# Optimization experiments

Hardware: AMD Instinct MI355X
Metric: run time of the kernel (lower is better)

## Reference

```python
import jax, jax.numpy as jnp
import numpy as np

K = 20  # max object ids (ids 1..K); masks value 0 = background
EPS_GN = 1e-5

def _conv3(x, w, b):
    # 3x3 conv, padding=1 == SAME, NCHW/OIHW
    y = jax.lax.conv_general_dilated(x, w, (1, 1), 'SAME',
                                     dimension_numbers=('NCHW', 'OIHW', 'NCHW'))
    return y + b[None, :, None, None]

def _groupnorm(x, groups, w, b):
    B, C, H, W = x.shape
    xg = x.reshape(B, groups, C // groups, H, W)
    m = xg.mean(axis=(2, 3, 4), keepdims=True)
    v = xg.var(axis=(2, 3, 4), keepdims=True)
    xn = ((xg - m) * jax.lax.rsqrt(v + EPS_GN)).reshape(B, C, H, W)
    return xn * w[None, :, None, None] + b[None, :, None, None]


def setup_inputs() -> dict:
    key = jax.random.key(0)
    ks = jax.random.split(key, 8)
    def p(k, shape, s=0.05):
        return jax.random.normal(k, shape, jnp.float32) * s
    return {
        'x': jax.random.normal(ks[0], (4, 512, 128, 128), jnp.float32),
        'masks': jax.random.randint(ks[1], (4, 128, 128), 0, 21, jnp.int32),
        'w1': p(ks[2], (256, 512, 3, 3)), 'b1': jnp.zeros((256,), jnp.float32),
        'g1w': jnp.ones((256,), jnp.float32), 'g1b': jnp.zeros((256,), jnp.float32),
        'w2': p(ks[3], (128, 256, 3, 3)), 'b2': jnp.zeros((128,), jnp.float32),
        'g2w': jnp.ones((128,), jnp.float32), 'g2b': jnp.zeros((128,), jnp.float32),
        'w3': p(ks[4], (64, 128, 3, 3)), 'b3': jnp.zeros((64,), jnp.float32),
        'g3w': jnp.ones((64,), jnp.float32), 'g3b': jnp.zeros((64,), jnp.float32),
        'wb': p(ks[5], (7, 64)), 'bb': jnp.zeros((7,), jnp.float32),
        'wc': p(ks[6], (1, 64)), 'bc': jnp.zeros((1,), jnp.float32),
    }


def reference(x, masks, w1, b1, g1w, g1b, w2, b2, g2w, g2b,
              w3, b3, g3w, g3b, wb, bb, wc, bc):
    # encoder: (conv3 -> GN -> relu) x3
    h = jax.nn.relu(_groupnorm(_conv3(x, w1, b1), 8, g1w, g1b))
    h = jax.nn.relu(_groupnorm(_conv3(h, w2, b2), 4, g2w, g2b))
    h = jax.nn.relu(_groupnorm(_conv3(h, w3, b3), 4, g3w, g3b))  # [B,64,H,W]

    # masked segment-mean pooling over all ids 1..K (vectorized unique-loop)
    ids = jnp.arange(1, K + 1, dtype=masks.dtype)
    onehot = (masks[:, None, :, :] == ids[None, :, None, None]).astype(h.dtype)  # [B,K,H,W]
    sums = jnp.einsum('bchw,bkhw->bkc', h, onehot)          # [B,K,64]
    counts = onehot.sum(axis=(2, 3))                        # [B,K]
    pooled = sums / (counts[..., None] + 1e-6)              # [B,K,64]

    # 1x1 conv heads on pooled vector == dense matmuls
    boxes = jnp.einsum('bkc,oc->bko', pooled, wb) + bb      # [B,K,7]
    scores = jax.nn.sigmoid(jnp.einsum('bkc,oc->bko', pooled, wc) + bc)[..., 0]  # [B,K]
    return (boxes, scores)
```

## Files before the change

### kernel.cpp

```cpp
#include <hip/hip_runtime.h>
#include <hip/hip_bf16.h>
#include <math.h>

#define HW 16384
#define BATCH 4
#define KIDS 20

using short8 = __attribute__((ext_vector_type(8))) short;
using f32x4  = __attribute__((ext_vector_type(4))) float;

__device__ __forceinline__ unsigned short bfbits(float f) {
  __hip_bfloat16 h = __float2bfloat16(f);
  return *(unsigned short*)&h;
}

__device__ __forceinline__ void gload_lds16(const void* g, void* l) {
  __builtin_amdgcn_global_load_lds(
      (const __attribute__((address_space(1))) void*)g,
      (__attribute__((address_space(3))) void*)l, 16, 0, 0);
}

__global__ __launch_bounds__(256) void zero_k(float* __restrict__ p, int n) {
  int i = blockIdx.x*256 + threadIdx.x;
  if (i < n) p[i] = 0.f;
}

__global__ __launch_bounds__(256) void x_to_nhwc_k(const float* __restrict__ in,
                                                   __hip_bfloat16* __restrict__ out)
{
  __shared__ float tile[32][65];
  int t = blockIdx.x;
  const int pxt = t & 255; t >>= 8;
  const int ct  = t & 15;  t >>= 4;
  const int b   = t;
  const int tid = threadIdx.x;
  #pragma unroll
  for (int it = 0; it < 8; ++it) {
    int idx = tid + it*256;
    int px_l = idx & 63, c_l = idx >> 6;
    tile[c_l][px_l] = in[((size_t)(b*512 + ct*32 + c_l))*HW + pxt*64 + px_l];
  }
  __syncthreads();
  #pragma unroll
  for (int it = 0; it < 4; ++it) {
    int idx = tid + it*256;
    int c2 = idx & 15, px_l = idx >> 4;
    unsigned u = ((unsigned)bfbits(tile[c2*2+1][px_l]) << 16) | bfbits(tile[c2*2][px_l]);
    *(unsigned*)(out + ((size_t)(b*HW + pxt*64 + px_l))*512 + ct*32 + c2*2) = u;
  }
}

template<int Co, int Ci>
__global__ __launch_bounds__(256) void pack_w_k(const float* __restrict__ w,
                                                __hip_bfloat16* __restrict__ out)
{
  const int i = blockIdx.x*256 + threadIdx.x;
  const int ci = i & (Ci-1);
  const int r  = i >> __builtin_ctz(Ci);
  const int co = r & (Co-1);
  const int t  = r >> __builtin_ctz(Co);
  out[i] = __float2bfloat16(w[((size_t)co*Ci + ci)*9 + t]);
}

template<int Ci, int Co, int CPG, int MT>
__global__ __launch_bounds__(512, 2) void conv_mfma_k(
    const __hip_bfloat16* __restrict__ xin,
    const __hip_bfloat16* __restrict__ wpk,
    const float* __restrict__ bias,
    float* __restrict__ out,
    float* __restrict__ partS, float* __restrict__ partSS)
{
  constexpr int ROWS = 2, NT = 4, SR = 4, RG = 64;
  constexpr int WCO = 2*MT*16;
  constexpr int NC  = Ci/32;
  constexpr int NGW = (MT*16)/CPG;
  constexpr int IB  = SR*130*32;
  constexpr int UW  = 9*WCO/16;
  __shared__ __align__(16) short lds[2*IB + 9*WCO*32];
  short* const wlds = lds + 2*IB;

  const int b  = blockIdx.x / RG;
  const int r0 = (blockIdx.x % RG) * ROWS;
  const int co0 = blockIdx.y * WCO;
  const int tid = threadIdx.x;
  const int wave = tid >> 6, lane = tid & 63;
  const int row_w = wave & 1;
  const int pw    = (wave >> 1) & 1;
  const int coh   = wave >> 2;
  const int co_w  = co0 + coh*MT*16;
  const int y = r0 + row_w;
  const int lr = lane & 15, q = lane >> 4;
  const int ls = lane >> 2, lq = lane & 3;

  if (tid < 64) {
    int q16 = tid & 3, u = tid >> 2;
    int side = u & 1, r = (u >> 1) & 3, buf = u >> 3;
    short8 z = {0,0,0,0,0,0,0,0};
    *(short8*)(lds + buf*IB + (r*130 + (side ? 129 : 0))*32 + q16*8) = z;
  }
  if (r0 == 0) {
    short8 z = {0,0,0,0,0,0,0,0};
    for (int i = tid; i < 2*520; i += 512) {
      int buf = i / 520, j = i % 520;
      *((short8*)(lds + buf*IB) + j) = z;
    }
  }
  if (r0 == 126) {
    short8 z = {0,0,0,0,0,0,0,0};
    for (int i = tid; i < 2*520; i += 512) {
      int buf = i / 520, j = i % 520;
      *((short8*)(lds + buf*IB + (SR-1)*130*32) + j) = z;
    }
  }

  const size_t in_base = (size_t)b * HW * Ci;
  auto stage_i = [&](int buf, int ci0) {
    #pragma unroll
    for (int it = 0; it < 4; ++it) {
      int gi = wave*4 + it;
      int r = gi >> 3, seg = gi & 7;
      int yy = r0 + r - 1;
      if ((unsigned)yy < 128u)
        gload_lds16(xin + in_base + (size_t)(yy*128 + seg*16 + ls)*Ci + ci0 + lq*8,
                    lds + buf*IB + (r*130 + seg*16 + 1)*32);
    }
  };
  auto stage_w = [&](int ci0) {
    for (int u = wave; u < UW; u += 8) {
      int t = u / (WCO/16), cb = u % (WCO/16);
      gload_lds16(wpk + ((size_t)(t*Co + co0 + cb*16 + ls))*Ci + ci0 + lq*8,
                  wlds + (t*WCO + cb*16)*32);
    }
  };

  f32x4 acc[MT][NT] = {};
  stage_i(0, 0);
  __syncthreads();
  int cur = 0;
  for (int c = 0; c < NC; ++c) {
    const int ci0 = c*32;
    stage_w(ci0);
    if (c+1 < NC) {
      stage_i(cur^1, ci0 + 32);
      asm volatile("s_waitcnt vmcnt(4)" ::: "memory");
    } else {
      asm volatile("s_waitcnt vmcnt(0)" ::: "memory");
    }
    __builtin_amdgcn_s_barrier();
    __builtin_amdgcn_sched_barrier(0);
    const short* ib = lds + cur*IB;
    #pragma unroll
    for (int t = 0; t < 9; ++t) {
      const int dy = t/3, dx = t%3;
      short8 af[MT], bf[NT];
      #pragma unroll
      for (int mt = 0; mt < MT; ++mt)
        af[mt] = *(const short8*)(wlds + (t*WCO + coh*MT*16 + mt*16 + lr)*32 + q*8);
      #pragma unroll
      for (int nt = 0; nt < NT; ++nt)
        bf[nt] = *(const short8*)(ib + ((row_w+dy)*130 + pw*64 + nt*16 + lr + dx)*32 + q*8);
      #pragma unroll
      for (int mt = 0; mt < MT; ++mt)
        #pragma unroll
        for (int nt = 0; nt < NT; ++nt)
          acc[mt][nt] = __builtin_amdgcn_mfma_f32_16x16x32_bf16(
              af[mt], bf[nt], acc[mt][nt], 0, 0, 0);
    }
    __builtin_amdgcn_s_barrier();
    cur ^= 1;
  }

  float sg[NGW] = {}, ssg[NGW] = {};
  #pragma unroll
  for (int mt = 0; mt < MT; ++mt) {
    const int g = (mt*16) / CPG;
    #pragma unroll
    for (int nt = 0; nt < NT; ++nt) {
      int px = pw*64 + nt*16 + lr;
      int co = co_w + mt*16 + q*4;
      const float4 bv = *(const float4*)(bias + co);
      f32x4 v = acc[mt][nt];
      v[0] += bv.x; v[1] += bv.y; v[2] += bv.z; v[3] += bv.w;
      sg[g]  += v[0] + v[1] + v[2] + v[3];
      ssg[g] += v[0]*v[0] + v[1]*v[1] + v[2]*v[2] + v[3]*v[3];
      *(f32x4*)(out + ((size_t)(b*HW + y*128 + px))*Co + co) = v;
    }
  }
  const int bgbase = b*(Co/CPG) + co_w/CPG;
  #pragma unroll
  for (int g = 0; g < NGW; ++g) {
    float s = sg[g], ss = ssg[g];
    #pragma unroll
    for (int off = 32; off; off >>= 1) {
      s  += __shfl_xor(s, off);
      ss += __shfl_xor(ss, off);
    }
    if (lane == 0) {
      atomicAdd(&partS[bgbase + g], s);
      atomicAdd(&partSS[bgbase + g], ss);
    }
  }
}

__global__ void gn_final_k(const float* __restrict__ partS,
                           const float* __restrict__ partSS,
                           float* __restrict__ mv, int nbg, float inv_n)
{
  const int i = threadIdx.x;
  if (i < nbg) {
    float s = partS[i], ss = partSS[i];
    float mean = s*inv_n, var = ss*inv_n - mean*mean;
    mv[2*i] = mean; mv[2*i+1] = rsqrtf(var + 1e-5f);
  }
}

template<int C, int CPG, bool BF16OUT>
__global__ __launch_bounds__(256) void gn_apply_k(const float* __restrict__ in,
    const float* __restrict__ mv, const float* __restrict__ gw,
    const float* __restrict__ gb, void* __restrict__ outp)
{
  constexpr int C4 = C/4;
  constexpr int G = C/CPG;
  const int i = blockIdx.x*256 + threadIdx.x;
  const int c4 = i & (C4-1);
  const int pxb = i >> __builtin_ctz(C4);
  const int b = pxb >> 14;
  const int c = c4*4;
  const int bg = b*G + c/CPG;
  const float mean = mv[2*bg], inv = mv[2*bg+1];
  float4 v = *((const float4*)in + i);
  const float4 w4 = *(const float4*)(gw + c);
  const float4 b4 = *(const float4*)(gb + c);
  float r0 = fmaxf((v.x-mean)*inv*w4.x + b4.x, 0.f);
  float r1 = fmaxf((v.y-mean)*inv*w4.y + b4.y, 0.f);
  float r2 = fmaxf((v.z-mean)*inv*w4.z + b4.z, 0.f);
  float r3 = fmaxf((v.w-mean)*inv*w4.w + b4.w, 0.f);
  if (BF16OUT) {
    uint2 o;
    o.x = ((unsigned)bfbits(r1) << 16) | bfbits(r0);
    o.y = ((unsigned)bfbits(r3) << 16) | bfbits(r2);
    *(uint2*)((__hip_bfloat16*)outp + (size_t)i*4) = o;
  } else {
    *((float4*)outp + i) = make_float4(r0,r1,r2,r3);
  }
}

__global__ __launch_bounds__(256) void pool_counts_k(
    const int* __restrict__ masks, float* __restrict__ counts)
{
  __shared__ int hist[KIDS];
  const int b = blockIdx.x;
  if (threadIdx.x < KIDS) hist[threadIdx.x] = 0;
  __syncthreads();
  for (int p = threadIdx.x; p < HW; p += 256) {
    const int m = masks[b*HW + p];
    if (m > 0) atomicAdd(&hist[m-1], 1);
  }
  __syncthreads();
  if (threadIdx.x < KIDS) counts[b*KIDS + threadIdx.x] = (float)hist[threadIdx.x];
}

__global__ __launch_bounds__(256) void pool_sums_k(const float* __restrict__ h3,
    const int* __restrict__ masks, float* __restrict__ sums)
{
  __shared__ float acc[KIDS*64];
  const int b = blockIdx.x >> 5, chunk = blockIdx.x & 31;
  const int tid = threadIdx.x;
  for (int j = tid; j < KIDS*64; j += 256) acc[j] = 0.f;
  __syncthreads();
  const int ch = tid & 63, pi = tid >> 6;
  const int p0 = chunk*512;
  for (int p = p0 + pi; p < p0 + 512; p += 4) {
    int m = masks[b*HW + p];
    if (m > 0) atomicAdd(&acc[(m-1)*64 + ch], h3[((size_t)(b*HW + p))*64 + ch]);
  }
  __syncthreads();
  for (int j = tid; j < KIDS*64; j += 256) atomicAdd(&sums[b*KIDS*64 + j], acc[j]);
}

__global__ __launch_bounds__(64) void heads_k(
    const float* __restrict__ sums, const float* __restrict__ counts,
    const float* __restrict__ wb, const float* __restrict__ bb,
    const float* __restrict__ wc, const float* __restrict__ bc,
    float* __restrict__ out)
{
  const int bk = blockIdx.x;
  const int c = threadIdx.x;
  const float pooled = sums[bk*64 + c] / (counts[bk] + 1e-6f);
  #pragma unroll
  for (int o = 0; o < 7; ++o) {
    float t = pooled * wb[o*64 + c];
    for (int off = 32; off > 0; off >>= 1) t += __shfl_down(t, off);
    if (c == 0) out[bk*7 + o] = t + bb[o];
  }
  float t = pooled * wc[c];
  for (int off = 32; off > 0; off >>= 1) t += __shfl_down(t, off);
  if (c == 0) out[BATCH*KIDS*7 + bk] = 1.f / (1.f + expf(-(t + bc[0])));
}

extern "C" void kernel_launch(void* const* d_in, const int* in_sizes, int n_in,
                              void* d_out, int out_size, void* d_ws, size_t ws_size,
                              hipStream_t stream)
{
  const float* x     = (const float*)d_in[0];
  const int*   masks = (const int*)  d_in[1];
  const float* w1 = (const float*)d_in[2];
  const float* b1 = (const float*)d_in[3];
  const float* g1w= (const float*)d_in[4];
  const float* g1b= (const float*)d_in[5];
  const float* w2 = (const float*)d_in[6];
  const float* b2 = (const float*)d_in[7];
  const float* g2w= (const float*)d_in[8];
  const float* g2b= (const float*)d_in[9];
  const float* w3 = (const float*)d_in[10];
  const float* b3 = (const float*)d_in[11];
  const float* g3w= (const float*)d_in[12];
  const float* g3b= (const float*)d_in[13];
  const float* wb = (const float*)d_in[14];
  const float* bb = (const float*)d_in[15];
  const float* wc = (const float*)d_in[16];
  const float* bc = (const float*)d_in[17];
  float* out = (float*)d_out;

  char* ws = (char*)d_ws;
  __hip_bfloat16* xb  = (__hip_bfloat16*)ws;
  __hip_bfloat16* h1b = (__hip_bfloat16*)ws;
  __hip_bfloat16* h2b = (__hip_bfloat16*)(ws + (size_t)(32<<20));
  float*          h3  = (float*)         (ws + (size_t)(48<<20));
  float* c1 = (float*)(ws + (size_t)(64<<20));
  float* c2 = c1;
  float* c3 = (float*)(ws + (size_t)(96<<20));
  __hip_bfloat16* wp1 = (__hip_bfloat16*)(ws + (size_t)(128<<20));
  __hip_bfloat16* wp2 = wp1 + 9*256*512;
  __hip_bfloat16* wp3 = wp2 + 9*128*256;
  char* tail = (char*)(wp3 + 9*64*128);
  float* mv     = (float*)tail;
  float* partS  = mv + 64;
  float* partSS = partS + 64;
  float* sums   = partSS + 64;
  float* counts = sums + 5120;

  zero_k<<<21, 256, 0, stream>>>(partS, 64 + 64 + 5120);

  x_to_nhwc_k<<<16384, 256, 0, stream>>>(x, xb);
  pack_w_k<256,512><<<4608, 256, 0, stream>>>(w1, wp1);
  pack_w_k<128,256><<<1152, 256, 0, stream>>>(w2, wp2);
  pack_w_k< 64,128><<< 288, 256, 0, stream>>>(w3, wp3);

  conv_mfma_k<512,256,32,4><<<dim3(256,2), 512, 0, stream>>>(
      xb, wp1, b1, c1, partS, partSS);
  gn_final_k<<<1, 64, 0, stream>>>(partS, partSS, mv, 32, 1.f/(32.f*HW));
  gn_apply_k<256,32,true><<<16384, 256, 0, stream>>>(c1, mv, g1w, g1b, h1b);

  conv_mfma_k<256,128,32,4><<<dim3(256,1), 512, 0, stream>>>(
      h1b, wp2, b2, c2, partS + 32, partSS + 32);
  gn_final_k<<<1, 64, 0, stream>>>(partS + 32, partSS + 32, mv, 16, 1.f/(32.f*HW));
  gn_apply_k<128,32,true><<<8192, 256, 0, stream>>>(c2, mv, g2w, g2b, h2b);

  conv_mfma_k<128,64,16,2><<<dim3(256,1), 512, 0, stream>>>(
      h2b, wp3, b3, c3, partS + 48, partSS + 48);
  gn_final_k<<<1, 64, 0, stream>>>(partS + 48, partSS + 48, mv, 16, 1.f/(16.f*HW));
  gn_apply_k<64,16,false><<<4096, 256, 0, stream>>>(c3, mv, g3w, g3b, h3);

  pool_counts_k<<<BATCH, 256, 0, stream>>>(masks, counts);
  pool_sums_k<<<BATCH*32, 256, 0, stream>>>(h3, masks, sums);
  heads_k<<<BATCH*KIDS, 64, 0, stream>>>(sums, counts, wb, bb, wc, bc, out);
}
```

Baseline: 706.0 us.

## Re-layout conv LDS tiles in 16-pixel segments and double-buffer MFMA fragments

Changes the shared-memory layout of the input and weight tiles to 512-short segments indexed by lane-major (lr, q) so fragment reads avoid bank conflicts. Out-of-bounds rows are now redirected to a trash LDS slot instead of skipped, which keeps the issued load count uniform. The per-tap fragment loads are software-pipelined with a two-slot register buffer so the next tap's LDS reads overlap the current MFMAs. This uses more registers, which may affect occupancy at the 2-waves-per-SIMD launch bound.

Measured after the change: 747.8 us. +5.9%, slower.

```diff
diff --git a/kernel.cpp b/kernel.cpp
--- a/kernel.cpp
+++ b/kernel.cpp
@@ -70,17 +70,20 @@
     float* __restrict__ out,
     float* __restrict__ partS, float* __restrict__ partSS)
 {
-  constexpr int ROWS = 2, NT = 4, SR = 4, RG = 64;
-  constexpr int WCO = 2*MT*16;
+  constexpr int NT  = 4;
+  constexpr int RG  = 64;
   constexpr int NC  = Ci/32;
   constexpr int NGW = (MT*16)/CPG;
-  constexpr int IB  = SR*130*32;
-  constexpr int UW  = 9*WCO/16;
-  __shared__ __align__(16) short lds[2*IB + 9*WCO*32];
-  short* const wlds = lds + 2*IB;
+  constexpr int WCO = 2*MT*16;
+  constexpr int WSEG = WCO/16;
+  constexpr int IBs = 4*10*512;
+  constexpr int WLs = 9*WSEG*512;
+  __shared__ __align__(16) short lds[2*IBs + WLs + 512];
+  short* const wlds  = lds + 2*IBs;
+  short* const trash = lds + 2*IBs + WLs;
 
   const int b  = blockIdx.x / RG;
-  const int r0 = (blockIdx.x % RG) * ROWS;
+  const int r0 = (blockIdx.x % RG) * 2;
   const int co0 = blockIdx.y * WCO;
   const int tid = threadIdx.x;
   const int wave = tid >> 6, lane = tid & 63;
@@ -90,48 +93,60 @@
   const int co_w  = co0 + coh*MT*16;
   const int y = r0 + row_w;
   const int lr = lane & 15, q = lane >> 4;
-  const int ls = lane >> 2, lq = lane & 3;
-
-  if (tid < 64) {
-    int q16 = tid & 3, u = tid >> 2;
-    int side = u & 1, r = (u >> 1) & 3, buf = u >> 3;
+  const int ls = lane & 15, lq = lane >> 4;
+
+  {
     short8 z = {0,0,0,0,0,0,0,0};
-    *(short8*)(lds + buf*IB + (r*130 + (side ? 129 : 0))*32 + q16*8) = z;
-  }
-  if (r0 == 0) {
-    short8 z = {0,0,0,0,0,0,0,0};
-    for (int i = tid; i < 2*520; i += 512) {
-      int buf = i / 520, j = i % 520;
-      *((short8*)(lds + buf*IB) + j) = z;
-    }
-  }
-  if (r0 == 126) {
-    short8 z = {0,0,0,0,0,0,0,0};
-    for (int i = tid; i < 2*520; i += 512) {
-      int buf = i / 520, j = i % 520;
-      *((short8*)(lds + buf*IB + (SR-1)*130*32) + j) = z;
+    for (int i = tid; i < 1024; i += 512) {
+      int u = i >> 6, m = i & 63;
+      int buf = u >> 3, r = (u >> 1) & 3, side = u & 1;
+      *((short8*)(lds + buf*IBs + r*5120 + side*9*512) + m) = z;
+    }
+    if (r0 == 0) {
+      for (int i = tid; i < 2*640; i += 512) {
+        int buf = i / 640, m = i % 640;
+        *((short8*)(lds + buf*IBs + 0*5120) + m) = z;
+      }
+    }
+    if (r0 == 126) {
+      for (int i = tid; i < 2*640; i += 512) {
+        int buf = i / 640, m = i % 640;
+        *((short8*)(lds + buf*IBs + 3*5120) + m) = z;
+      }
     }
   }
 
   const size_t in_base = (size_t)b * HW * Ci;
+
   auto stage_i = [&](int buf, int ci0) {
     #pragma unroll
     for (int it = 0; it < 4; ++it) {
       int gi = wave*4 + it;
-      int r = gi >> 3, seg = gi & 7;
+      int r = gi >> 3, sd = (gi & 7) + 1;
       int yy = r0 + r - 1;
-      if ((unsigned)yy < 128u)
-        gload_lds16(xin + in_base + (size_t)(yy*128 + seg*16 + ls)*Ci + ci0 + lq*8,
-                    lds + buf*IB + (r*130 + seg*16 + 1)*32);
+      bool ok = (unsigned)yy < 128u;
+      int yc = ok ? yy : 0;
+      const __hip_bfloat16* src = xin + in_base
+          + (size_t)(yc*128 + (sd-1)*16 + ls)*Ci + ci0 + lq*8;
+      short* dst = ok ? (lds + buf*IBs + r*5120 + sd*512) : trash;
+      gload_lds16(src, dst);
     }
   };
   auto stage_w = [&](int ci0) {
-    for (int u = wave; u < UW; u += 8) {
-      int t = u / (WCO/16), cb = u % (WCO/16);
-      gload_lds16(wpk + ((size_t)(t*Co + co0 + cb*16 + ls))*Ci + ci0 + lq*8,
-                  wlds + (t*WCO + cb*16)*32);
+    for (int u = wave; u < 9*WSEG; u += 8) {
+      int t = u / WSEG, cs = u % WSEG;
+      gload_lds16(wpk + ((size_t)(t*Co + co0 + cs*16 + ls))*Ci + ci0 + lq*8,
+                  wlds + u*512);
     }
   };
+
+  int base_dx[3];
+  #pragma unroll
+  for (int dx = 0; dx < 3; ++dx) {
+    int e = dx + 15 + lr;
+    base_dx[dx] = row_w*5120 + pw*2048 + (e>>4)*512 + (e&15)*8 + q*128;
+  }
+  const int base_a = coh*MT*512 + q*128 + lr*8;
 
   f32x4 acc[MT][NT] = {};
   stage_i(0, 0);
@@ -148,23 +163,35 @@
     }
     __builtin_amdgcn_s_barrier();
     __builtin_amdgcn_sched_barrier(0);
-    const short* ib = lds + cur*IB;
+    const short* ib = lds + cur*IBs;
+
+    short8 af[2][MT], bf[2][NT];
+    #pragma unroll
+    for (int mt = 0; mt < MT; ++mt)
+      af[0][mt] = *(const short8*)(wlds + base_a + mt*512);
+    #pragma unroll
+    for (int nt = 0; nt < NT; ++nt)
+      bf[0][nt] = *(const short8*)(ib + base_dx[0] + nt*512);
+
     #pragma unroll
     for (int t = 0; t < 9; ++t) {
-      const int dy = t/3, dx = t%3;
-      short8 af[MT], bf[NT];
-      #pragma unroll
-      for (int mt = 0; mt < MT; ++mt)
-        af[mt] = *(const short8*)(wlds + (t*WCO + coh*MT*16 + mt*16 + lr)*32 + q*8);
-      #pragma unroll
-      for (int nt = 0; nt < NT; ++nt)
-        bf[nt] = *(const short8*)(ib + ((row_w+dy)*130 + pw*64 + nt*16 + lr + dx)*32 + q*8);
+      const int cb = t & 1, nb = cb ^ 1;
+      if (t < 8) {
+        const int t1 = t + 1, dy1 = t1/3, dx1 = t1%3;
+        const short* wt = wlds + t1*WSEG*512;
+        #pragma unroll
+        for (int mt = 0; mt < MT; ++mt)
+          af[nb][mt] = *(const short8*)(wt + base_a + mt*512);
+        #pragma unroll
+        for (int nt = 0; nt < NT; ++nt)
+          bf[nb][nt] = *(const short8*)(ib + base_dx[dx1] + dy1*5120 + nt*512);
+      }
       #pragma unroll
       for (int mt = 0; mt < MT; ++mt)
         #pragma unroll
         for (int nt = 0; nt < NT; ++nt)
           acc[mt][nt] = __builtin_amdgcn_mfma_f32_16x16x32_bf16(
-              af[mt], bf[nt], acc[mt][nt], 0, 0, 0);
+              af[cb][mt], bf[cb][nt], acc[mt][nt], 0, 0, 0);
     }
     __builtin_amdgcn_s_barrier();
     cur ^= 1;
```
